# Kernel tuning notes

Measured on AMD Instinct MI355X. Metric: run time of the kernel, lower is better.

## Reference

```python
import jax, jax.numpy as jnp
import numpy as np

N = 50000      # nodes
E = 800000     # edges (avg degree 16)
D_IN = 128     # in_feats
D_OUT = 128    # out_feats
EPS = 1e-5     # LayerNorm eps


def setup_inputs() -> dict:
    key = jax.random.key(0)
    ks = jax.random.split(key, 8)
    stdv = 1.0 / np.sqrt(5 * D_IN)
    return {
        "h": jax.random.normal(ks[0], (N, D_IN), dtype=jnp.float32),
        "dist": jax.random.uniform(ks[1], (E,), dtype=jnp.float32),
        "W": jax.random.uniform(ks[2], (D_OUT, 5 * D_IN), minval=-stdv, maxval=stdv, dtype=jnp.float32),
        "b": jax.random.uniform(ks[3], (D_OUT,), minval=-stdv, maxval=stdv, dtype=jnp.float32),
        "gamma": jnp.ones((D_OUT,), dtype=jnp.float32),
        "beta": jnp.zeros((D_OUT,), dtype=jnp.float32),
        "src": jax.random.randint(ks[4], (E,), 0, N, dtype=jnp.int32),
        "dst": jax.random.randint(ks[5], (E,), 0, N, dtype=jnp.int32),
        "positions": jax.random.randint(ks[6], (E,), 0, 4, dtype=jnp.int32),
    }


def reference(h, dist, W, b, gamma, beta, src, dst, positions):
    n = h.shape[0]
    h_src = h[src]  # [E, D] gather once, reused by all four directions

    def direction(p):
        # edge-masked u_mul_e + sum aggregation to dst
        w = jnp.where(positions == p, dist, 0.0)
        return jax.ops.segment_sum(h_src * w[:, None], dst, num_segments=n)

    r = direction(0)   # right
    bt = direction(1)  # bottom
    l = direction(2)   # left
    t = direction(0)   # top (original code reuses positions == 0 — faithful)

    cat = jnp.concatenate([h, r, bt, l, t], axis=1)  # [N, 5D]
    z = cat @ W.T + b                                 # [N, D_OUT]
    mu = jnp.mean(z, axis=-1, keepdims=True)
    var = jnp.mean(jnp.square(z - mu), axis=-1, keepdims=True)
    z = (z - mu) * jax.lax.rsqrt(var + EPS) * gamma + beta
    return jax.nn.relu(z)
```

## Files before the change

### kernel.cpp

```cpp
#include <hip/hip_runtime.h>
#include <math.h>
#include <stdint.h>

constexpr int NN = 50000;
constexpr int EE = 800000;
constexpr int D  = 128;
constexpr int CAP = 64;
constexpr int BM = 32;
constexpr int NBX = (NN + BM - 1) / BM;

typedef __attribute__((ext_vector_type(8)))  short bf16x8;
typedef __attribute__((ext_vector_type(16))) float f32x16;

__device__ inline unsigned short f2bf(float x) {
    unsigned u = __builtin_bit_cast(unsigned, x);
    unsigned r = (u + 0x7FFF + ((u >> 16) & 1)) >> 16;
    return (unsigned short)r;
}
__device__ inline float bf2f(unsigned short b) {
    unsigned u = ((unsigned)b) << 16;
    return __builtin_bit_cast(float, u);
}

__global__ __launch_bounds__(256) void prep_wfrag(const float* __restrict__ W,
                                                  unsigned short* __restrict__ Wfh,
                                                  unsigned short* __restrict__ Wfl)
{
    int tid = blockIdx.x * 256 + threadIdx.x;
    int ln  = tid & 31;
    int hs  = (tid >> 5) & 1;
    int s   = (tid >> 6) & 7;
    int vcb = tid >> 9;
    int oc  = vcb * 32 + ln;
    short h8[8], l8[8];
#pragma unroll
    for (int j = 0; j < 8; ++j) {
        int k = s * 16 + hs * 8 + j;
        float v;
        if (oc < 128)      v = W[oc * 640 + k];
        else if (oc < 256) v = W[(oc - 128) * 640 + 128 + k]
                             + W[(oc - 128) * 640 + 512 + k];
        else if (oc < 384) v = W[(oc - 256) * 640 + 256 + k];
        else               v = W[(oc - 384) * 640 + 384 + k];
        unsigned short hb = f2bf(v);
        h8[j] = (short)hb;
        l8[j] = (short)f2bf(v - bf2f(hb));
    }
    *(bf16x8*)(Wfh + (size_t)tid * 8) = *(bf16x8*)h8;
    *(bf16x8*)(Wfl + (size_t)tid * 8) = *(bf16x8*)l8;
}

__global__ __launch_bounds__(256) void fill_bucket(const int* __restrict__ src,
                                                   const int* __restrict__ dst,
                                                   const int* __restrict__ pos,
                                                   const float* __restrict__ dist,
                                                   int* __restrict__ deg,
                                                   int2* __restrict__ bucket)
{
    int e = blockIdx.x * 256 + threadIdx.x;
    if (e >= EE) return;
    int p = pos[e];
    if (p == 3) return;
    int d_ = dst[e];
    int slot = atomicAdd(&deg[d_], 1);
    if (slot < CAP)
        bucket[(size_t)d_ * CAP + slot] =
            make_int2(src[e] * 3 + p, __float_as_int(dist[e]));
}

__global__ __launch_bounds__(256, 4) void pre_gemm(
    const float* __restrict__ h,
    const unsigned short* __restrict__ Wfh, const unsigned short* __restrict__ Wfl,
    const float* __restrict__ bias,
    float* __restrict__ base, unsigned short* __restrict__ Y)
{
    __shared__ __align__(16) short Af[16 * 32 * 8];

    const int t = threadIdx.x;
    const int lane = t & 63;
    const int w = t >> 6;
    const int ln = lane & 31;
    const int hs = lane >> 5;
    const int node0 = blockIdx.x * BM;
    const int by = blockIdx.y;

    {
        int row = t >> 3;
        int g   = t & 7;
        int node = node0 + row;
        float ff[16];
        if (node < NN) {
            const float* hp = h + (size_t)node * D + g * 16;
            float4 f0 = *(const float4*)hp;
            float4 f1 = *(const float4*)(hp + 4);
            float4 f2 = *(const float4*)(hp + 8);
            float4 f3 = *(const float4*)(hp + 12);
            ff[0]=f0.x; ff[1]=f0.y; ff[2]=f0.z; ff[3]=f0.w;
            ff[4]=f1.x; ff[5]=f1.y; ff[6]=f1.z; ff[7]=f1.w;
            ff[8]=f2.x; ff[9]=f2.y; ff[10]=f2.z; ff[11]=f2.w;
            ff[12]=f3.x; ff[13]=f3.y; ff[14]=f3.z; ff[15]=f3.w;
        } else {
#pragma unroll
            for (int j = 0; j < 16; ++j) ff[j] = 0.f;
        }
        short b16[16];
#pragma unroll
        for (int j = 0; j < 16; ++j) b16[j] = (short)f2bf(ff[j]);
        int s0 = 2 * g, s1 = 2 * g + 1;
        *(bf16x8*)(Af + (s0 * 32 + (row ^ s0)) * 8) = *(bf16x8*)&b16[0];
        *(bf16x8*)(Af + (s1 * 32 + (row ^ s1)) * 8) = *(bf16x8*)&b16[8];
    }
    __syncthreads();

    const int vcb = by * 4 + w;

    auto LOADB = [&](int s, bf16x8& bh, bf16x8& bl) {
        size_t fo = ((size_t)((vcb * 8 + s) * 2 + hs) * 32 + ln) * 8;
        bh = *(const bf16x8*)(Wfh + fo);
        bl = *(const bf16x8*)(Wfl + fo);
    };
    auto LOADA = [&](int s) -> bf16x8 {
        int sl = s * 2 + hs;
        return *(const bf16x8*)(Af + (sl * 32 + (ln ^ sl)) * 8);
    };

    f32x16 acc;
#pragma unroll
    for (int i = 0; i < 16; ++i) acc[i] = 0.f;

    bf16x8 bh0, bl0, bh1, bl1;
    LOADB(0, bh0, bl0);
#pragma unroll
    for (int s = 0; s < 8; s += 2) {
        if (s + 1 < 8) LOADB(s + 1, bh1, bl1);
        bf16x8 aa = LOADA(s);
        __builtin_amdgcn_s_setprio(1);
        acc = __builtin_amdgcn_mfma_f32_32x32x16_bf16(aa, bh0, acc, 0, 0, 0);
        acc = __builtin_amdgcn_mfma_f32_32x32x16_bf16(aa, bl0, acc, 0, 0, 0);
        __builtin_amdgcn_s_setprio(0);
        if (s + 2 < 8) LOADB(s + 2, bh0, bl0);
        aa = LOADA(s + 1);
        __builtin_amdgcn_s_setprio(1);
        acc = __builtin_amdgcn_mfma_f32_32x32x16_bf16(aa, bh1, acc, 0, 0, 0);
        acc = __builtin_amdgcn_mfma_f32_32x32x16_bf16(aa, bl1, acc, 0, 0, 0);
        __builtin_amdgcn_s_setprio(0);
    }

    int vc = by * 128 + w * 32 + ln;
#pragma unroll
    for (int reg = 0; reg < 16; ++reg) {
        int rl = (reg & 3) + 8 * (reg >> 2) + 4 * hs;
        int grow = node0 + rl;
        if (grow < NN) {
            if (by == 0)
                base[(size_t)grow * D + vc] = acc[reg] + bias[vc];
            else
                Y[(size_t)grow * 384 + (vc - 128)] = f2bf(acc[reg]);
        }
    }
}

__global__ __launch_bounds__(256, 8) void agg_ln(
    const unsigned short* __restrict__ Y, const float* __restrict__ base,
    const int2* __restrict__ bucket, const int* __restrict__ deg,
    const float* __restrict__ gamma, const float* __restrict__ beta,
    float* __restrict__ out)
{
    int w = threadIdx.x >> 6;
    int node = blockIdx.x * 4 + w;
    if (node >= NN) return;
    int lane = threadIdx.x & 63;
    int ln = lane & 31;
    int hs = lane >> 5;

    int n = deg[node];
    if (n > CAP) n = CAP;
    int2 mreg = (lane < n) ? bucket[(size_t)node * CAP + lane] : make_int2(0, 0);

    float a[4] = {0.f, 0.f, 0.f, 0.f};
    for (int b0 = 0; b0 < n; b0 += 16) {
        ushort4 v[8];
        float   wq[8];
#pragma unroll
        for (int j = 0; j < 8; ++j) {
            int idx = b0 + 2 * j + hs;
            int s3 = __shfl(mreg.x, idx, 64);
            int wy = __shfl(mreg.y, idx, 64);
            wq[j] = __int_as_float(wy);
            v[j] = *(const ushort4*)(Y + (size_t)s3 * D + ln * 4);
        }
#pragma unroll
        for (int j = 0; j < 8; ++j) {
            a[0] = fmaf(bf2f(v[j].x), wq[j], a[0]);
            a[1] = fmaf(bf2f(v[j].y), wq[j], a[1]);
            a[2] = fmaf(bf2f(v[j].z), wq[j], a[2]);
            a[3] = fmaf(bf2f(v[j].w), wq[j], a[3]);
        }
    }
#pragma unroll
    for (int c = 0; c < 4; ++c) a[c] += __shfl_xor(a[c], 32, 64);

    float4 bv = *(const float4*)(base + (size_t)node * D + ln * 4);
    float z[4] = {bv.x + a[0], bv.y + a[1], bv.z + a[2], bv.w + a[3]};

    float s = z[0] + z[1] + z[2] + z[3];
    float ss = z[0]*z[0] + z[1]*z[1] + z[2]*z[2] + z[3]*z[3];
#pragma unroll
    for (int m = 1; m < 32; m <<= 1) {
        s  += __shfl_xor(s, m, 64);
        ss += __shfl_xor(ss, m, 64);
    }
    float mu  = s * (1.f / 128.f);
    float var = ss * (1.f / 128.f) - mu * mu;
    float rs  = rsqrtf(var + 1e-5f);

    if (hs == 0) {
        float4 g4 = *(const float4*)(gamma + ln * 4);
        float4 b4 = *(const float4*)(beta + ln * 4);
        float o[4];
        o[0] = (z[0] - mu) * rs * g4.x + b4.x;
        o[1] = (z[1] - mu) * rs * g4.y + b4.y;
        o[2] = (z[2] - mu) * rs * g4.z + b4.z;
        o[3] = (z[3] - mu) * rs * g4.w + b4.w;
#pragma unroll
        for (int c = 0; c < 4; ++c) o[c] = o[c] > 0.f ? o[c] : 0.f;
        *(float4*)(out + (size_t)node * D + ln * 4) = *(float4*)o;
    }
}

extern "C" void kernel_launch(void* const* d_in, const int* in_sizes, int n_in,
                              void* d_out, int out_size, void* d_ws, size_t ws_size,
                              hipStream_t stream)
{
    const float* h     = (const float*)d_in[0];
    const float* dist  = (const float*)d_in[1];
    const float* W     = (const float*)d_in[2];
    const float* bias  = (const float*)d_in[3];
    const float* gamma = (const float*)d_in[4];
    const float* beta  = (const float*)d_in[5];
    const int*   src   = (const int*)d_in[6];
    const int*   dst   = (const int*)d_in[7];
    const int*   pos   = (const int*)d_in[8];

    unsigned short* Wfh  = (unsigned short*)d_ws;
    unsigned short* Wfl  = Wfh + 8192 * 8;
    unsigned short* Y    = Wfl + 8192 * 8;
    float*          base = (float*)(Y + (size_t)NN * 384);
    int*            deg  = (int*)(base + (size_t)NN * D);
    int2* bucket = (int2*)(((uintptr_t)(deg + NN) + 15) & ~(uintptr_t)15);

    hipMemsetAsync(deg, 0, NN * sizeof(int), stream);

    prep_wfrag<<<32, 256, 0, stream>>>(W, Wfh, Wfl);
    fill_bucket<<<(EE + 255) / 256, 256, 0, stream>>>(src, dst, pos, dist, deg, bucket);
    pre_gemm<<<dim3(NBX, 4), 256, 0, stream>>>(h, Wfh, Wfl, bias, base, Y);
    agg_ln<<<(NN + 3) / 4, 256, 0, stream>>>(Y, base, bucket, deg, gamma, beta,
                                             (float*)d_out);
}
```

Baseline: 190.9 us.

## Stage GEMM output through LDS for coalesced stores and store base as bf16

The pre-GEMM epilogue now writes its MFMA accumulators into shared memory and then stores each row with wide, contiguous 8-byte writes, replacing scattered 2- and 4-byte stores. The self term (base) is stored as bf16 with the bias folded in, which halves its write and later read traffic in agg_ln. Launch bounds are raised to 8 waves per SIMD for occupancy. The bf16 base adds rounding error before LayerNorm, and the extra LDS round trip adds two barriers.

```diff
diff --git a/kernel.cpp b/kernel.cpp
--- a/kernel.cpp
+++ b/kernel.cpp
@@ -68,11 +68,11 @@
             make_int2(src[e] * 3 + p, __float_as_int(dist[e]));
 }
 
-__global__ __launch_bounds__(256, 4) void pre_gemm(
+__global__ __launch_bounds__(256, 8) void pre_gemm(
     const float* __restrict__ h,
     const unsigned short* __restrict__ Wfh, const unsigned short* __restrict__ Wfl,
     const float* __restrict__ bias,
-    float* __restrict__ base, unsigned short* __restrict__ Y)
+    unsigned short* __restrict__ baseB, unsigned short* __restrict__ Y)
 {
     __shared__ __align__(16) short Af[16 * 32 * 8];
 
@@ -145,23 +145,42 @@
         acc = __builtin_amdgcn_mfma_f32_32x32x16_bf16(aa, bl1, acc, 0, 0, 0);
         __builtin_amdgcn_s_setprio(0);
     }
-
-    int vc = by * 128 + w * 32 + ln;
-#pragma unroll
-    for (int reg = 0; reg < 16; ++reg) {
-        int rl = (reg & 3) + 8 * (reg >> 2) + 4 * hs;
-        int grow = node0 + rl;
+    __syncthreads();
+
+    {
+        float bc = (by == 0) ? bias[w * 32 + ln] : 0.f;
+        unsigned short* Cs = (unsigned short*)Af;
+#pragma unroll
+        for (int reg = 0; reg < 16; ++reg) {
+            int rl = (reg & 3) + 8 * (reg >> 2) + 4 * hs;
+            Cs[rl * 128 + w * 32 + ln] = f2bf(acc[reg] + bc);
+        }
+    }
+    __syncthreads();
+
+    {
+        const unsigned short* Cs = (const unsigned short*)Af;
+        int row = t >> 3;
+        int g   = t & 7;
+        int grow = node0 + row;
         if (grow < NN) {
-            if (by == 0)
-                base[(size_t)grow * D + vc] = acc[reg] + bias[vc];
-            else
-                Y[(size_t)grow * 384 + (vc - 128)] = f2bf(acc[reg]);
+            uint2 u0 = *(const uint2*)(Cs + row * 128 + g * 16);
+            uint2 u1 = *(const uint2*)(Cs + row * 128 + g * 16 + 4);
+            uint2 u2 = *(const uint2*)(Cs + row * 128 + g * 16 + 8);
+            uint2 u3 = *(const uint2*)(Cs + row * 128 + g * 16 + 12);
+            unsigned short* dp = (by == 0)
+                ? baseB + (size_t)grow * D + g * 16
+                : Y + ((size_t)grow * 3 + (by - 1)) * D + g * 16;
+            *(uint2*)(dp)      = u0;
+            *(uint2*)(dp + 4)  = u1;
+            *(uint2*)(dp + 8)  = u2;
+            *(uint2*)(dp + 12) = u3;
         }
     }
 }
 
 __global__ __launch_bounds__(256, 8) void agg_ln(
-    const unsigned short* __restrict__ Y, const float* __restrict__ base,
+    const unsigned short* __restrict__ Y, const unsigned short* __restrict__ baseB,
     const int2* __restrict__ bucket, const int* __restrict__ deg,
     const float* __restrict__ gamma, const float* __restrict__ beta,
     float* __restrict__ out)
@@ -200,8 +219,9 @@
 #pragma unroll
     for (int c = 0; c < 4; ++c) a[c] += __shfl_xor(a[c], 32, 64);
 
-    float4 bv = *(const float4*)(base + (size_t)node * D + ln * 4);
-    float z[4] = {bv.x + a[0], bv.y + a[1], bv.z + a[2], bv.w + a[3]};
+    ushort4 bv = *(const ushort4*)(baseB + (size_t)node * D + ln * 4);
+    float z[4] = {bf2f(bv.x) + a[0], bf2f(bv.y) + a[1],
+                  bf2f(bv.z) + a[2], bf2f(bv.w) + a[3]};
 
     float s = z[0] + z[1] + z[2] + z[3];
     float ss = z[0]*z[0] + z[1]*z[1] + z[2]*z[2] + z[3]*z[3];
@@ -242,18 +262,18 @@
     const int*   dst   = (const int*)d_in[7];
     const int*   pos   = (const int*)d_in[8];
 
-    unsigned short* Wfh  = (unsigned short*)d_ws;
-    unsigned short* Wfl  = Wfh + 8192 * 8;
-    unsigned short* Y    = Wfl + 8192 * 8;
-    float*          base = (float*)(Y + (size_t)NN * 384);
-    int*            deg  = (int*)(base + (size_t)NN * D);
+    unsigned short* Wfh   = (unsigned short*)d_ws;
+    unsigned short* Wfl   = Wfh + 8192 * 8;
+    unsigned short* Y     = Wfl + 8192 * 8;
+    unsigned short* baseB = Y + (size_t)NN * 3 * D;
+    int*            deg   = (int*)(baseB + (size_t)NN * D);
     int2* bucket = (int2*)(((uintptr_t)(deg + NN) + 15) & ~(uintptr_t)15);
 
     hipMemsetAsync(deg, 0, NN * sizeof(int), stream);
 
     prep_wfrag<<<32, 256, 0, stream>>>(W, Wfh, Wfl);
     fill_bucket<<<(EE + 255) / 256, 256, 0, stream>>>(src, dst, pos, dist, deg, bucket);
-    pre_gemm<<<dim3(NBX, 4), 256, 0, stream>>>(h, Wfh, Wfl, bias, base, Y);
-    agg_ln<<<(NN + 3) / 4, 256, 0, stream>>>(Y, base, bucket, deg, gamma, beta,
+    pre_gemm<<<dim3(NBX, 4), 256, 0, stream>>>(h, Wfh, Wfl, bias, baseB, Y);
+    agg_ln<<<(NN + 3) / 4, 256, 0, stream>>>(Y, baseB, bucket, deg, gamma, beta,
                                              (float*)d_out);
 }
```

Result: faster. 185.8 us (-2.7%).
